# Kernel optimization log

Hardware: AMD Instinct MI355X
Metric: run time of the kernel (lower is better)

## Reference

```python
import jax, jax.numpy as jnp
import numpy as np

SAT_LO, SAT_HI = -1.0, 1.0  # args_dict['saturations']


def setup_inputs() -> dict:
    key = jax.random.key(0)
    ks = jax.random.split(key, 6)
    B, T, n = 256, 512, 1024
    std = 1.0 / np.sqrt(n)
    x = jax.random.normal(ks[0], (B, T), jnp.float32)
    state0 = jnp.zeros((n,), jnp.float32)
    mask = jnp.ones((n,), jnp.float32)
    # 2x2 recurrent mixing matrix, scaled roughly to spectral radius ~init_radius
    w = 0.9 * jax.random.normal(ks[1], (2, 2), jnp.float32) * std * np.sqrt(n)
    dec_orth = jax.random.normal(ks[2], (n,), jnp.float32) * std
    enc_orth = jax.random.normal(ks[3], (n,), jnp.float32) * std
    decoder = jax.random.normal(ks[4], (n,), jnp.float32) * std
    encoder = jax.random.normal(ks[5], (n,), jnp.float32) * std
    return {"x": x, "state0": state0, "mask": mask, "w": w,
            "dec_orth": dec_orth, "enc_orth": enc_orth,
            "decoder": decoder, "encoder": encoder}


def reference(x, state0, mask, w, dec_orth, enc_orth, decoder, encoder):
    # W = sum_ij w[i,j] * v_i (x) v_j with v_0 = dec_orth, v_1 = enc_orth  -> [n, n]
    W = (w[0, 0] * jnp.outer(dec_orth, dec_orth)
         + w[0, 1] * jnp.outer(dec_orth, enc_orth)
         + w[1, 0] * jnp.outer(enc_orth, dec_orth)
         + w[1, 1] * jnp.outer(enc_orth, enc_orth))
    B = x.shape[0]
    n = state0.shape[0]
    s0 = jnp.zeros((B, n), x.dtype) + state0  # broadcast init state to batch

    def step(s, xt):
        # external current: encoder * x_t  -> [B, n]
        pre = (s + mask * (encoder * xt[:, None])) @ W.T
        s_new = mask * jnp.clip(pre, SAT_LO, SAT_HI)
        out = s_new @ decoder  # [B]
        return s_new, out

    _, outs = jax.lax.scan(step, s0, x.T)  # outs: [T, B]
    return outs.T  # [B, T]
```

## Files before the change

### kernel.cpp

```cpp
#include <hip/hip_runtime.h>


typedef float f32x2 __attribute__((ext_vector_type(2)));

constexpr int Bc = 256;
constexpr int Tc = 512;
constexpr int CH = Tc / 64;

__device__ __forceinline__ float readlane_f(float v, int l) {
    return __int_as_float(__builtin_amdgcn_readlane(__float_as_int(v), l));
}

__device__ __forceinline__ f32x2 pk_fma(f32x2 a, f32x2 b, f32x2 c) {
    f32x2 d;
    asm("v_pk_fma_f32 %0, %1, %2, %3" : "=v"(d) : "v"(a), "v"(b), "v"(c));
    return d;
}
__device__ __forceinline__ f32x2 pk_mul(f32x2 a, f32x2 b) {
    f32x2 d;
    asm("v_pk_mul_f32 %0, %1, %2" : "=v"(d) : "v"(a), "v"(b));
    return d;
}

#define DPP3(lvl, msk)                                                                              \
        "v_add_f32_dpp %[a], %[a], %[a] " lvl " row_mask:" msk " bank_mask:0xf bound_ctrl:1\n\t"    \
        "v_add_f32_dpp %[b], %[b], %[b] " lvl " row_mask:" msk " bank_mask:0xf bound_ctrl:1\n\t"    \
        "v_add_f32_dpp %[c], %[c], %[c] " lvl " row_mask:" msk " bank_mask:0xf bound_ctrl:1\n\t"

#define WAVE_REDUCE3_READ(h1, h2, h3, s1, s2, s3)                                                   \
    asm("s_nop 1\n\t"                                                                               \
        DPP3("row_shr:1",   "0xf")                                                                  \
        DPP3("row_shr:2",   "0xf")                                                                  \
        DPP3("row_shr:4",   "0xf")                                                                  \
        DPP3("row_shr:8",   "0xf")                                                                  \
        DPP3("row_bcast:15","0xa")                                                                  \
        DPP3("row_bcast:31","0xc")                                                                  \
        "v_readlane_b32 %[x], %[a], 63\n\t"                                                         \
        "v_readlane_b32 %[y], %[b], 63\n\t"                                                         \
        "v_readlane_b32 %[z], %[c], 63"                                                             \
        : [a] "+v"(h1), [b] "+v"(h2), [c] "+v"(h3),                                                 \
          [x] "=s"(s1), [y] "=s"(s2), [z] "=s"(s3))

#define DECL_TBL(i) f32x2 d2_##i, e2_##i, g1_##i, g2_##i, wo_##i

#define INIT_TBL(i) do { \
    _Pragma("unroll") \
    for (int h = 0; h < 2; ++h) { \
        const int c = lane + 64 * (2 * (i) + h); \
        const float dv   = dec_orth[c]; \
        const float ev   = enc_orth[c]; \
        const float mv   = mask[c]; \
        const float encv = encoder[c]; \
        const float decv = decoder[c]; \
        const float s0v  = state0[c]; \
        const float mdv = mv * dv, mev = mv * ev; \
        d2_##i[h]  = dv;  e2_##i[h]  = ev; \
        g1_##i[h] = fmaf(w00, mdv, w01 * mev); \
        g2_##i[h] = fmaf(w10, mdv, w11 * mev); \
        wo_##i[h] = mv * decv; \
        s0d += s0v * dv;  s0e += s0v * ev; \
        kd = fmaf(mv * encv, dv, kd); \
        ke = fmaf(mv * encv, ev, ke); \
    } \
} while (0)

#define ACC_J(i) do { \
    f32x2 tt = pk_fma(b2, e2_##i, pk_mul(a2, d2_##i)); \
    f32x2 mm; \
    mm.x = __builtin_amdgcn_fmed3f(tt.x, -1.0f, 1.0f); \
    mm.y = __builtin_amdgcn_fmed3f(tt.y, -1.0f, 1.0f); \
    p1 = pk_fma(mm, g1_##i, p1); \
    p2 = pk_fma(mm, g2_##i, p2); \
    po = pk_fma(mm, wo_##i, po); \
} while (0)

#define ACC_J0(i) do { \
    f32x2 tt = pk_fma(b2, e2_##i, pk_mul(a2, d2_##i)); \
    f32x2 mm; \
    mm.x = __builtin_amdgcn_fmed3f(tt.x, -1.0f, 1.0f); \
    mm.y = __builtin_amdgcn_fmed3f(tt.y, -1.0f, 1.0f); \
    p1 = pk_mul(mm, g1_##i); \
    p2 = pk_mul(mm, g2_##i); \
    po = pk_mul(mm, wo_##i); \
} while (0)

__global__ __attribute__((amdgpu_waves_per_eu(1, 1))) __launch_bounds__(64)
void twotwonet_kernel(
    const float* __restrict__ x,
    const float* __restrict__ state0,
    const float* __restrict__ mask,
    const float* __restrict__ w,
    const float* __restrict__ dec_orth,
    const float* __restrict__ enc_orth,
    const float* __restrict__ decoder,
    const float* __restrict__ encoder,
    float* __restrict__ out)
{
    const int b    = blockIdx.x;
    const int lane = threadIdx.x;

    const float w00 = w[0], w01 = w[1], w10 = w[2], w11 = w[3];

    DECL_TBL(0); DECL_TBL(1); DECL_TBL(2); DECL_TBL(3);
    DECL_TBL(4); DECL_TBL(5); DECL_TBL(6); DECL_TBL(7);

    float s0d = 0.f, s0e = 0.f, kd = 0.f, ke = 0.f;
    INIT_TBL(0); INIT_TBL(1); INIT_TBL(2); INIT_TBL(3);
    INIT_TBL(4); INIT_TBL(5); INIT_TBL(6); INIT_TBL(7);

#pragma unroll
    for (int m = 32; m >= 1; m >>= 1) {
        s0d += __shfl_xor(s0d, m, 64);
        s0e += __shfl_xor(s0e, m, 64);
        kd  += __shfl_xor(kd, m, 64);
        ke  += __shfl_xor(ke, m, 64);
    }

    const float A1 = fmaf(w00, kd, w01 * ke);
    const float A2 = fmaf(w10, kd, w11 * ke);

    const float* xrow = x + (size_t)b * Tc;
    float xr[CH];
#pragma unroll
    for (int c = 0; c < CH; ++c) xr[c] = xrow[lane + 64 * c];

    float q1 = fmaf(w00, s0d, w01 * s0e);
    float q2 = fmaf(w10, s0d, w11 * s0e);

#pragma unroll
    for (int c = 0; c < CH; ++c) {
        float obuf = 0.f;
#pragma unroll 2
        for (int t2 = 0; t2 < 64; ++t2) {
            const float xs = readlane_f(xr[c], t2);

            const float al = fmaf(xs, A1, q1);
            const float be = fmaf(xs, A2, q2);
            const f32x2 a2 = {al, al};
            const f32x2 b2 = {be, be};

            f32x2 p1, p2, po;
            ACC_J0(0);
            ACC_J(1); ACC_J(2); ACC_J(3);
            ACC_J(4); ACC_J(5); ACC_J(6); ACC_J(7);

            float h1 = p1.x + p1.y;
            float h2 = p2.x + p2.y;
            float ho = po.x + po.y;

            float r1, r2, ro;
            WAVE_REDUCE3_READ(h1, h2, ho, r1, r2, ro);
            q1 = r1;
            q2 = r2;

            obuf = (t2 == lane) ? ro : obuf;
        }
        out[(size_t)b * Tc + 64 * c + lane] = obuf;
    }
}

extern "C" void kernel_launch(void* const* d_in, const int* in_sizes, int n_in,
                              void* d_out, int out_size, void* d_ws, size_t ws_size,
                              hipStream_t stream) {
    const float* x        = (const float*)d_in[0];
    const float* state0   = (const float*)d_in[1];
    const float* mask     = (const float*)d_in[2];
    const float* w        = (const float*)d_in[3];
    const float* dec_orth = (const float*)d_in[4];
    const float* enc_orth = (const float*)d_in[5];
    const float* decoder  = (const float*)d_in[6];
    const float* encoder  = (const float*)d_in[7];
    float* out = (float*)d_out;

    twotwonet_kernel<<<dim3(Bc), dim3(64), 0, stream>>>(
        x, state0, mask, w, dec_orth, enc_orth, decoder, encoder, out);
}
```

Before: 101.2 us.

## Skip per-element recurrence when no saturation can occur, using rank-2 closed form

At setup, the kernel precomputes the 2x2 projected dynamics: the projections of the gain vectors onto dec_orth and enc_orth, the decoder projections, and the maximum absolute masked basis entries. Each step checks a conservative bound that rules out clipping. When it holds, the kernel updates the two scalar state coordinates and the output with a few FMAs, skipping the 1024-element elementwise pass and the wave reduction. Otherwise it falls back to the exact clipped path. This trades a cheap ballot and bound check per step for removing the serial DPP reduction chain, with small rounding differences from the reassociated sums.

```diff
diff --git a/kernel.cpp b/kernel.cpp
--- a/kernel.cpp
+++ b/kernel.cpp
@@ -55,12 +55,19 @@
         const float s0v  = state0[c]; \
         const float mdv = mv * dv, mev = mv * ev; \
         d2_##i[h]  = dv;  e2_##i[h]  = ev; \
-        g1_##i[h] = fmaf(w00, mdv, w01 * mev); \
-        g2_##i[h] = fmaf(w10, mdv, w11 * mev); \
-        wo_##i[h] = mv * decv; \
+        const float g1v = fmaf(w00, mdv, w01 * mev); \
+        const float g2v = fmaf(w10, mdv, w11 * mev); \
+        const float wov = mv * decv; \
+        g1_##i[h] = g1v;  g2_##i[h] = g2v;  wo_##i[h] = wov; \
         s0d += s0v * dv;  s0e += s0v * ev; \
         kd = fmaf(mv * encv, dv, kd); \
         ke = fmaf(mv * encv, ev, ke); \
+        pd1 = fmaf(dv, g1v, pd1);  pe1 = fmaf(ev, g1v, pe1); \
+        pd2 = fmaf(dv, g2v, pd2);  pe2 = fmaf(ev, g2v, pe2); \
+        od  = fmaf(dv, wov, od);   oe  = fmaf(ev, wov, oe); \
+        const float dabs = (mv != 0.f) ? fabsf(dv) : 0.f; \
+        const float eabs = (mv != 0.f) ? fabsf(ev) : 0.f; \
+        dm = fmaxf(dm, dabs);  em = fmaxf(em, eabs); \
     } \
 } while (0)
 
@@ -105,6 +112,8 @@
     DECL_TBL(4); DECL_TBL(5); DECL_TBL(6); DECL_TBL(7);
 
     float s0d = 0.f, s0e = 0.f, kd = 0.f, ke = 0.f;
+    float pd1 = 0.f, pe1 = 0.f, pd2 = 0.f, pe2 = 0.f, od = 0.f, oe = 0.f;
+    float dm = 0.f, em = 0.f;
     INIT_TBL(0); INIT_TBL(1); INIT_TBL(2); INIT_TBL(3);
     INIT_TBL(4); INIT_TBL(5); INIT_TBL(6); INIT_TBL(7);
 
@@ -114,15 +123,27 @@
         s0e += __shfl_xor(s0e, m, 64);
         kd  += __shfl_xor(kd, m, 64);
         ke  += __shfl_xor(ke, m, 64);
+        pd1 += __shfl_xor(pd1, m, 64);
+        pe1 += __shfl_xor(pe1, m, 64);
+        pd2 += __shfl_xor(pd2, m, 64);
+        pe2 += __shfl_xor(pe2, m, 64);
+        od  += __shfl_xor(od, m, 64);
+        oe  += __shfl_xor(oe, m, 64);
+        dm = fmaxf(dm, __shfl_xor(dm, m, 64));
+        em = fmaxf(em, __shfl_xor(em, m, 64));
     }
 
     const float A1 = fmaf(w00, kd, w01 * ke);
     const float A2 = fmaf(w10, kd, w11 * ke);
 
     const float* xrow = x + (size_t)b * Tc;
-    float xr[CH];
+    float xr1[CH], xr2[CH];
 #pragma unroll
-    for (int c = 0; c < CH; ++c) xr[c] = xrow[lane + 64 * c];
+    for (int c = 0; c < CH; ++c) {
+        const float xv = xrow[lane + 64 * c];
+        xr1[c] = xv * A1;
+        xr2[c] = xv * A2;
+    }
 
     float q1 = fmaf(w00, s0d, w01 * s0e);
     float q2 = fmaf(w10, s0d, w11 * s0e);
@@ -132,26 +153,33 @@
         float obuf = 0.f;
 #pragma unroll 2
         for (int t2 = 0; t2 < 64; ++t2) {
-            const float xs = readlane_f(xr[c], t2);
-
-            const float al = fmaf(xs, A1, q1);
-            const float be = fmaf(xs, A2, q2);
-            const f32x2 a2 = {al, al};
-            const f32x2 b2 = {be, be};
-
-            f32x2 p1, p2, po;
-            ACC_J0(0);
-            ACC_J(1); ACC_J(2); ACC_J(3);
-            ACC_J(4); ACC_J(5); ACC_J(6); ACC_J(7);
-
-            float h1 = p1.x + p1.y;
-            float h2 = p2.x + p2.y;
-            float ho = po.x + po.y;
-
-            float r1, r2, ro;
-            WAVE_REDUCE3_READ(h1, h2, ho, r1, r2, ro);
-            q1 = r1;
-            q2 = r2;
+            const float al = q1 + readlane_f(xr1[c], t2);
+            const float be = q2 + readlane_f(xr2[c], t2);
+
+            float ro;
+            const float chk = fmaf(fabsf(be), em, fabsf(al) * dm);
+            if (__ballot(chk <= 1.0f) == ~0ull) {
+                q1 = fmaf(be, pe1, al * pd1);
+                q2 = fmaf(be, pe2, al * pd2);
+                ro = fmaf(be, oe,  al * od);
+            } else {
+                const f32x2 a2 = {al, al};
+                const f32x2 b2 = {be, be};
+                f32x2 p1, p2, po;
+                ACC_J0(0);
+                ACC_J(1); ACC_J(2); ACC_J(3);
+                ACC_J(4); ACC_J(5); ACC_J(6); ACC_J(7);
+
+                float h1 = p1.x + p1.y;
+                float h2 = p2.x + p2.y;
+                float ho = po.x + po.y;
+
+                float r1, r2, r3;
+                WAVE_REDUCE3_READ(h1, h2, ho, r1, r2, r3);
+                q1 = r1;
+                q2 = r2;
+                ro = r3;
+            }
 
             obuf = (t2 == lane) ? ro : obuf;
         }
```

Result: slower. 133.6 us (+32.1%).

## Move output reduction off the recurrent critical path and prescale inputs

Applied to the files above, without the earlier changes.

Splits the per-step wave reduction so that only the two recurrence sums (q1, q2) go through the DPP reduction chain. The output dot product is computed during the DPP latency gaps and reduced afterwards, outside the dependency chain. The input x is premultiplied by A1/A2 so each step needs an add instead of an fma. Each step now issues a separate lane-63 global store in place of one buffered coalesced store per 64 steps. That adds memory traffic and extra DPP instructions after the critical path.

```diff
diff --git a/kernel.cpp b/kernel.cpp
--- a/kernel.cpp
+++ b/kernel.cpp
@@ -22,24 +22,42 @@
     return d;
 }
 
-#define DPP3(lvl, msk)                                                                              \
+#define DPP2(lvl, msk)                                                                              \
         "v_add_f32_dpp %[a], %[a], %[a] " lvl " row_mask:" msk " bank_mask:0xf bound_ctrl:1\n\t"    \
         "v_add_f32_dpp %[b], %[b], %[b] " lvl " row_mask:" msk " bank_mask:0xf bound_ctrl:1\n\t"    \
-        "v_add_f32_dpp %[c], %[c], %[c] " lvl " row_mask:" msk " bank_mask:0xf bound_ctrl:1\n\t"
+        "s_nop 0\n\t"
 
-#define WAVE_REDUCE3_READ(h1, h2, h3, s1, s2, s3)                                                   \
-    asm("s_nop 1\n\t"                                                                               \
-        DPP3("row_shr:1",   "0xf")                                                                  \
-        DPP3("row_shr:2",   "0xf")                                                                  \
-        DPP3("row_shr:4",   "0xf")                                                                  \
-        DPP3("row_shr:8",   "0xf")                                                                  \
-        DPP3("row_bcast:15","0xa")                                                                  \
-        DPP3("row_bcast:31","0xc")                                                                  \
+#define REDUCE_Q(h1, h2, poa, pob)                                                                  \
+    asm volatile("s_nop 1\n\t"                                                                      \
+        DPP2("row_shr:1",   "0xf")                                                                  \
+        DPP2("row_shr:2",   "0xf")                                                                  \
+        DPP2("row_shr:4",   "0xf")                                                                  \
+        DPP2("row_shr:8",   "0xf")                                                                  \
+        DPP2("row_bcast:15","0xa")                                                                  \
+        DPP2("row_bcast:31","0xc")                                                                  \
+        "s_nop 0"                                                                                   \
+        : [a] "+v"(h1), [b] "+v"(h2), [pa] "+v"(poa), [pb] "+v"(pob))
+
+#define READ_Q(h1, h2, s1, s2, dep)                                                                 \
+    asm volatile(                                                                                   \
         "v_readlane_b32 %[x], %[a], 63\n\t"                                                         \
-        "v_readlane_b32 %[y], %[b], 63\n\t"                                                         \
-        "v_readlane_b32 %[z], %[c], 63"                                                             \
-        : [a] "+v"(h1), [b] "+v"(h2), [c] "+v"(h3),                                                 \
-          [x] "=s"(s1), [y] "=s"(s2), [z] "=s"(s3))
+        "v_readlane_b32 %[y], %[b], 63"                                                             \
+        : [x] "=s"(s1), [y] "=s"(s2)                                                                \
+        : [a] "v"(h1), [b] "v"(h2), [d] "v"(dep))
+
+#define DPP1(lvl, msk)                                                                              \
+        "v_add_f32_dpp %[a], %[a], %[a] " lvl " row_mask:" msk " bank_mask:0xf bound_ctrl:1\n\t"    \
+        "s_nop 1\n\t"
+
+#define REDUCE_O(h)                                                                                 \
+    asm volatile("s_nop 1\n\t"                                                                      \
+        DPP1("row_shr:1",   "0xf")                                                                  \
+        DPP1("row_shr:2",   "0xf")                                                                  \
+        DPP1("row_shr:4",   "0xf")                                                                  \
+        DPP1("row_shr:8",   "0xf")                                                                  \
+        DPP1("row_bcast:15","0xa")                                                                  \
+        DPP1("row_bcast:31","0xc")                                                                  \
+        : [a] "+v"(h))
 
 #define DECL_TBL(i) f32x2 d2_##i, e2_##i, g1_##i, g2_##i, wo_##i
 
@@ -64,24 +82,12 @@
     } \
 } while (0)
 
-#define ACC_J(i) do { \
+#define ACC_P(i) do { \
     f32x2 tt = pk_fma(b2, e2_##i, pk_mul(a2, d2_##i)); \
-    f32x2 mm; \
-    mm.x = __builtin_amdgcn_fmed3f(tt.x, -1.0f, 1.0f); \
-    mm.y = __builtin_amdgcn_fmed3f(tt.y, -1.0f, 1.0f); \
-    p1 = pk_fma(mm, g1_##i, p1); \
-    p2 = pk_fma(mm, g2_##i, p2); \
-    po = pk_fma(mm, wo_##i, po); \
-} while (0)
-
-#define ACC_J0(i) do { \
-    f32x2 tt = pk_fma(b2, e2_##i, pk_mul(a2, d2_##i)); \
-    f32x2 mm; \
-    mm.x = __builtin_amdgcn_fmed3f(tt.x, -1.0f, 1.0f); \
-    mm.y = __builtin_amdgcn_fmed3f(tt.y, -1.0f, 1.0f); \
-    p1 = pk_mul(mm, g1_##i); \
-    p2 = pk_mul(mm, g2_##i); \
-    po = pk_mul(mm, wo_##i); \
+    mm_##i.x = __builtin_amdgcn_fmed3f(tt.x, -1.0f, 1.0f); \
+    mm_##i.y = __builtin_amdgcn_fmed3f(tt.y, -1.0f, 1.0f); \
+    p1 = pk_fma(mm_##i, g1_##i, p1); \
+    p2 = pk_fma(mm_##i, g2_##i, p2); \
 } while (0)
 
 __global__ __attribute__((amdgpu_waves_per_eu(1, 1))) __launch_bounds__(64)
@@ -120,42 +126,55 @@
     const float A2 = fmaf(w10, kd, w11 * ke);
 
     const float* xrow = x + (size_t)b * Tc;
-    float xr[CH];
+    float xr1[CH], xr2[CH];
 #pragma unroll
-    for (int c = 0; c < CH; ++c) xr[c] = xrow[lane + 64 * c];
+    for (int c = 0; c < CH; ++c) {
+        const float xv = xrow[lane + 64 * c];
+        xr1[c] = xv * A1;
+        xr2[c] = xv * A2;
+    }
 
     float q1 = fmaf(w00, s0d, w01 * s0e);
     float q2 = fmaf(w10, s0d, w11 * s0e);
 
+    float* outrow = out + (size_t)b * Tc;
+
 #pragma unroll
     for (int c = 0; c < CH; ++c) {
-        float obuf = 0.f;
 #pragma unroll 2
         for (int t2 = 0; t2 < 64; ++t2) {
-            const float xs = readlane_f(xr[c], t2);
-
-            const float al = fmaf(xs, A1, q1);
-            const float be = fmaf(xs, A2, q2);
+            const float al = q1 + readlane_f(xr1[c], t2);
+            const float be = q2 + readlane_f(xr2[c], t2);
             const f32x2 a2 = {al, al};
             const f32x2 b2 = {be, be};
 
-            f32x2 p1, p2, po;
-            ACC_J0(0);
-            ACC_J(1); ACC_J(2); ACC_J(3);
-            ACC_J(4); ACC_J(5); ACC_J(6); ACC_J(7);
+            f32x2 mm_0, mm_1, mm_2, mm_3, mm_4, mm_5, mm_6, mm_7;
+            f32x2 p1 = {0.f, 0.f}, p2 = {0.f, 0.f};
+            ACC_P(0); ACC_P(1); ACC_P(2); ACC_P(3);
+            ACC_P(4); ACC_P(5); ACC_P(6); ACC_P(7);
 
             float h1 = p1.x + p1.y;
             float h2 = p2.x + p2.y;
-            float ho = po.x + po.y;
 
-            float r1, r2, ro;
-            WAVE_REDUCE3_READ(h1, h2, ho, r1, r2, ro);
+            f32x2 poa = {0.f, 0.f}, pob = {0.f, 0.f};
+            REDUCE_Q(h1, h2, poa, pob);
+
+            poa = pk_fma(mm_0, wo_0, poa);  pob = pk_fma(mm_1, wo_1, pob);
+            poa = pk_fma(mm_2, wo_2, poa);  pob = pk_fma(mm_3, wo_3, pob);
+            poa = pk_fma(mm_4, wo_4, poa);  pob = pk_fma(mm_5, wo_5, pob);
+            poa = pk_fma(mm_6, wo_6, poa);  pob = pk_fma(mm_7, wo_7, pob);
+            const f32x2 pos = poa + pob;
+
+            float r1, r2;
+            READ_Q(h1, h2, r1, r2, pos);
             q1 = r1;
             q2 = r2;
 
-            obuf = (t2 == lane) ? ro : obuf;
+            float ho = pos.x + pos.y;
+            REDUCE_O(ho);
+
+            if (lane == 63) outrow[64 * c + t2] = ho;
         }
-        out[(size_t)b * Tc + 64 * c + lane] = obuf;
     }
 }
 
```

New measurement: 133.9 us. +32.3%, slower.

## Pack two batch rows per wave using half-wave butterfly reductions

Applied to the files above, without the earlier changes.

Each 64-lane wave now handles two batch rows, one per 32-lane half, with each lane holding twice as many state elements. The cross-lane reduction becomes a butterfly using DPP and ds_swizzle that keeps results in all lanes, removing readlane. Input x is broadcast per step through ds_bpermute with a one-step prefetch. The grid is halved, trading per-wave parallelism for fewer waves, so each serial step does more work per lane.

```diff
diff --git a/kernel.cpp b/kernel.cpp
--- a/kernel.cpp
+++ b/kernel.cpp
@@ -5,11 +5,7 @@
 
 constexpr int Bc = 256;
 constexpr int Tc = 512;
-constexpr int CH = Tc / 64;
-
-__device__ __forceinline__ float readlane_f(float v, int l) {
-    return __int_as_float(__builtin_amdgcn_readlane(__float_as_int(v), l));
-}
+constexpr int NCH = 16;
 
 __device__ __forceinline__ f32x2 pk_fma(f32x2 a, f32x2 b, f32x2 c) {
     f32x2 d;
@@ -22,31 +18,28 @@
     return d;
 }
 
-#define DPP3(lvl, msk)                                                                              \
-        "v_add_f32_dpp %[a], %[a], %[a] " lvl " row_mask:" msk " bank_mask:0xf bound_ctrl:1\n\t"    \
-        "v_add_f32_dpp %[b], %[b], %[b] " lvl " row_mask:" msk " bank_mask:0xf bound_ctrl:1\n\t"    \
-        "v_add_f32_dpp %[c], %[c], %[c] " lvl " row_mask:" msk " bank_mask:0xf bound_ctrl:1\n\t"
+template <int CTRL>
+__device__ __forceinline__ float bf_dpp(float v) {
+    int t = __builtin_amdgcn_update_dpp(0, __float_as_int(v), CTRL, 0xf, 0xf, true);
+    return v + __int_as_float(t);
+}
 
-#define WAVE_REDUCE3_READ(h1, h2, h3, s1, s2, s3)                                                   \
-    asm("s_nop 1\n\t"                                                                               \
-        DPP3("row_shr:1",   "0xf")                                                                  \
-        DPP3("row_shr:2",   "0xf")                                                                  \
-        DPP3("row_shr:4",   "0xf")                                                                  \
-        DPP3("row_shr:8",   "0xf")                                                                  \
-        DPP3("row_bcast:15","0xa")                                                                  \
-        DPP3("row_bcast:31","0xc")                                                                  \
-        "v_readlane_b32 %[x], %[a], 63\n\t"                                                         \
-        "v_readlane_b32 %[y], %[b], 63\n\t"                                                         \
-        "v_readlane_b32 %[z], %[c], 63"                                                             \
-        : [a] "+v"(h1), [b] "+v"(h2), [c] "+v"(h3),                                                 \
-          [x] "=s"(s1), [y] "=s"(s2), [z] "=s"(s3))
+#define BF5_3(h1, h2, h3) do {                                        \
+    h1 = bf_dpp<0xB1>(h1);  h2 = bf_dpp<0xB1>(h2);  h3 = bf_dpp<0xB1>(h3); \
+    h1 = bf_dpp<0x4E>(h1);  h2 = bf_dpp<0x4E>(h2);  h3 = bf_dpp<0x4E>(h3); \
+    h1 = bf_dpp<0x141>(h1); h2 = bf_dpp<0x141>(h2); h3 = bf_dpp<0x141>(h3); \
+    h1 = bf_dpp<0x140>(h1); h2 = bf_dpp<0x140>(h2); h3 = bf_dpp<0x140>(h3); \
+    h1 += __int_as_float(__builtin_amdgcn_ds_swizzle(__float_as_int(h1), 0x401F)); \
+    h2 += __int_as_float(__builtin_amdgcn_ds_swizzle(__float_as_int(h2), 0x401F)); \
+    h3 += __int_as_float(__builtin_amdgcn_ds_swizzle(__float_as_int(h3), 0x401F)); \
+} while (0)
 
 #define DECL_TBL(i) f32x2 d2_##i, e2_##i, g1_##i, g2_##i, wo_##i
 
 #define INIT_TBL(i) do { \
     _Pragma("unroll") \
     for (int h = 0; h < 2; ++h) { \
-        const int c = lane + 64 * (2 * (i) + h); \
+        const int c = l31 + 32 * (2 * (i) + h); \
         const float dv   = dec_orth[c]; \
         const float ev   = enc_orth[c]; \
         const float mv   = mask[c]; \
@@ -96,20 +89,27 @@
     const float* __restrict__ encoder,
     float* __restrict__ out)
 {
-    const int b    = blockIdx.x;
+    const int b0   = 2 * blockIdx.x;
     const int lane = threadIdx.x;
+    const int l31  = lane & 31;
+    const int half = lane >> 5;
+    const int h32x4 = (lane & 32) << 2;
 
     const float w00 = w[0], w01 = w[1], w10 = w[2], w11 = w[3];
 
-    DECL_TBL(0); DECL_TBL(1); DECL_TBL(2); DECL_TBL(3);
-    DECL_TBL(4); DECL_TBL(5); DECL_TBL(6); DECL_TBL(7);
+    DECL_TBL(0);  DECL_TBL(1);  DECL_TBL(2);  DECL_TBL(3);
+    DECL_TBL(4);  DECL_TBL(5);  DECL_TBL(6);  DECL_TBL(7);
+    DECL_TBL(8);  DECL_TBL(9);  DECL_TBL(10); DECL_TBL(11);
+    DECL_TBL(12); DECL_TBL(13); DECL_TBL(14); DECL_TBL(15);
 
     float s0d = 0.f, s0e = 0.f, kd = 0.f, ke = 0.f;
-    INIT_TBL(0); INIT_TBL(1); INIT_TBL(2); INIT_TBL(3);
-    INIT_TBL(4); INIT_TBL(5); INIT_TBL(6); INIT_TBL(7);
+    INIT_TBL(0);  INIT_TBL(1);  INIT_TBL(2);  INIT_TBL(3);
+    INIT_TBL(4);  INIT_TBL(5);  INIT_TBL(6);  INIT_TBL(7);
+    INIT_TBL(8);  INIT_TBL(9);  INIT_TBL(10); INIT_TBL(11);
+    INIT_TBL(12); INIT_TBL(13); INIT_TBL(14); INIT_TBL(15);
 
 #pragma unroll
-    for (int m = 32; m >= 1; m >>= 1) {
+    for (int m = 16; m >= 1; m >>= 1) {
         s0d += __shfl_xor(s0d, m, 64);
         s0e += __shfl_xor(s0e, m, 64);
         kd  += __shfl_xor(kd, m, 64);
@@ -119,43 +119,52 @@
     const float A1 = fmaf(w00, kd, w01 * ke);
     const float A2 = fmaf(w10, kd, w11 * ke);
 
-    const float* xrow = x + (size_t)b * Tc;
-    float xr[CH];
-#pragma unroll
-    for (int c = 0; c < CH; ++c) xr[c] = xrow[lane + 64 * c];
-
     float q1 = fmaf(w00, s0d, w01 * s0e);
     float q2 = fmaf(w10, s0d, w11 * s0e);
 
-#pragma unroll
-    for (int c = 0; c < CH; ++c) {
+    const float* xrow = x + (size_t)(b0 + half) * Tc;
+
+    for (int c = 0; c < NCH; ++c) {
+        const float xv = xrow[l31 + 32 * c];
+        const float xs1v = xv * A1;
+        const float xs2v = xv * A2;
+
+        float xs1 = __int_as_float(__builtin_amdgcn_ds_bpermute(h32x4, __float_as_int(xs1v)));
+        float xs2 = __int_as_float(__builtin_amdgcn_ds_bpermute(h32x4, __float_as_int(xs2v)));
+
         float obuf = 0.f;
 #pragma unroll 2
-        for (int t2 = 0; t2 < 64; ++t2) {
-            const float xs = readlane_f(xr[c], t2);
+        for (int t2 = 0; t2 < 32; ++t2) {
+            const int nt4 = (((t2 + 1) & 31) << 2) + h32x4;
+            const float xs1n = __int_as_float(__builtin_amdgcn_ds_bpermute(nt4, __float_as_int(xs1v)));
+            const float xs2n = __int_as_float(__builtin_amdgcn_ds_bpermute(nt4, __float_as_int(xs2v)));
 
-            const float al = fmaf(xs, A1, q1);
-            const float be = fmaf(xs, A2, q2);
+            const float al = q1 + xs1;
+            const float be = q2 + xs2;
             const f32x2 a2 = {al, al};
             const f32x2 b2 = {be, be};
 
             f32x2 p1, p2, po;
             ACC_J0(0);
-            ACC_J(1); ACC_J(2); ACC_J(3);
-            ACC_J(4); ACC_J(5); ACC_J(6); ACC_J(7);
+            ACC_J(1);  ACC_J(2);  ACC_J(3);
+            ACC_J(4);  ACC_J(5);  ACC_J(6);  ACC_J(7);
+            ACC_J(8);  ACC_J(9);  ACC_J(10); ACC_J(11);
+            ACC_J(12); ACC_J(13); ACC_J(14); ACC_J(15);
 
             float h1 = p1.x + p1.y;
             float h2 = p2.x + p2.y;
             float ho = po.x + po.y;
 
-            float r1, r2, ro;
-            WAVE_REDUCE3_READ(h1, h2, ho, r1, r2, ro);
-            q1 = r1;
-            q2 = r2;
+            BF5_3(h1, h2, ho);
 
-            obuf = (t2 == lane) ? ro : obuf;
+            q1 = h1;
+            q2 = h2;
+
+            obuf = (t2 == l31) ? ho : obuf;
+            xs1 = xs1n;
+            xs2 = xs2n;
         }
-        out[(size_t)b * Tc + 64 * c + lane] = obuf;
+        out[(size_t)(b0 + half) * Tc + 32 * c + l31] = obuf;
     }
 }
 
@@ -172,6 +181,6 @@
     const float* encoder  = (const float*)d_in[7];
     float* out = (float*)d_out;
 
-    twotwonet_kernel<<<dim3(Bc), dim3(64), 0, stream>>>(
+    twotwonet_kernel<<<dim3(Bc / 2), dim3(64), 0, stream>>>(
         x, state0, mask, w, dec_orth, enc_orth, decoder, encoder, out);
 }
```

Result: slower. 197.3 us (+95.1%).
